# Performance work log

Measured on AMD Instinct MI355X. Metric: run time of the kernel, lower is better.

Reference implementation:

```python
import jax, jax.numpy as jnp
import numpy as np

TWO_PI = 6.283185307179586


def setup_inputs() -> dict:
    key = jax.random.key(0)
    k1, k2, k3, k4, k5, k6 = jax.random.split(key, 6)
    B, T, D = 2, 8192, 1024
    x = jax.random.normal(k1, (B, T, D), dtype=jnp.float32)
    # nn.Linear weights are [out, in]; init with small scale like torch default
    s = 1.0 / np.sqrt(D)
    Wk = jax.random.uniform(k2, (D, D), jnp.float32, -s, s)
    Wv = jax.random.uniform(k3, (D, D), jnp.float32, -s, s)
    Wo = jax.random.uniform(k4, (D, D), jnp.float32, -s, s)
    # random phasor frequencies in [0, 2*pi)
    freqs = jax.random.uniform(k5, (D,), jnp.float32, 0.0, TWO_PI)
    return {"x": x, "Wk": Wk, "Wv": Wv, "Wo": Wo, "freqs": freqs}


def reference(x, Wk, Wv, Wo, freqs):
    B, T, C = x.shape
    # k projection is computed in the original forward but never used downstream
    k_real = x @ Wk.T  # [B,T,D] (dead value, kept for fidelity)
    v_real = x @ Wv.T  # [B,T,D]
    v = v_real.astype(jnp.complex64)
    # rotors: per-position unit phasors exp(i * t * freqs), shape [T, D]
    t = jnp.arange(T, dtype=jnp.float32)
    rotors = jnp.exp(1j * (t[:, None] * freqs[None, :])).astype(jnp.complex64)
    # bind each value with its rotor and accumulate causally (O(N) memory trace)
    memory_trace = jnp.cumsum(v * rotors[None, :, :], axis=1)  # [B,T,D] complex64
    # retrieve by unbinding with the conjugate rotor; take the real component
    retrieved = jnp.real(memory_trace * jnp.conj(rotors)[None, :, :])  # [B,T,D]
    return retrieved @ Wo.T
```

## Files before the change

kernel.cpp:

```cpp
#include <hip/hip_runtime.h>
#include <hip/hip_bf16.h>


#define B_  2
#define T_  8192
#define D_  1024
#define BT_ 16384
#define CS_ 64
#define NCHUNK_ 128

typedef __attribute__((ext_vector_type(4))) float f32x4;
typedef __attribute__((ext_vector_type(8))) short bf16x8;

static __device__ inline unsigned short f2bf(float f) {
    union { float f; unsigned int u; } a;
    a.f = f;
    unsigned int u = a.u;
    return (unsigned short)((u + 0x7FFFu + ((u >> 16) & 1u)) >> 16);
}
static __device__ inline float bf2f(unsigned short h) {
    union { unsigned int u; float f; } a;
    a.u = ((unsigned int)h) << 16;
    return a.f;
}

__global__ __launch_bounds__(256) void cast_all(const float* __restrict__ x,
                                                const float* __restrict__ Wv,
                                                const float* __restrict__ Wo,
                                                unsigned short* __restrict__ xb,
                                                unsigned short* __restrict__ wvb,
                                                unsigned short* __restrict__ wob) {
    const int nx = BT_ * D_ / 4;
    const int nw = D_ * D_ / 4;
    int i = blockIdx.x * 256 + threadIdx.x;
    const float4* src;
    unsigned short* dst;
    int j;
    if (i < nx)            { src = (const float4*)x;  dst = xb;  j = i; }
    else if (i < nx + nw)  { src = (const float4*)Wv; dst = wvb; j = i - nx; }
    else                   { src = (const float4*)Wo; dst = wob; j = i - nx - nw; }
    float4 v = src[j];
    ushort4 o;
    o.x = f2bf(v.x); o.y = f2bf(v.y); o.z = f2bf(v.z); o.w = f2bf(v.w);
    ((ushort4*)dst)[j] = o;
}

template <bool BF16OUT>
__global__ __launch_bounds__(256) void gemm_bt(const short* __restrict__ A,
                                               const short* __restrict__ Bm,
                                               void* __restrict__ Cout,
                                               int M, int N, int K) {
    __shared__ short lds[8192];
    const int lane = threadIdx.x & 63;
    const int wave = threadIdx.x >> 6;
    const int wr = wave >> 1, wc = wave & 1;

    const int nb = N >> 7;
    const int id = blockIdx.x;
    const int xcd = id & 7;
    const int slot = id >> 3;
    const int bn = (slot % nb) * 128;
    const int bm = (xcd * ((M >> 7) >> 3) + slot / nb) * 128;

    const int r0 = lane >> 2;
    const int cb = lane & 3;

    const int m_base = wr * 64 + (lane & 15);
    const int n_base = wc * 64 + (lane & 15);
    const int k_off = (lane >> 4) * 8;

    f32x4 acc[4][4] = {};

    for (int k0 = 0; k0 < K; k0 += 32) {
#pragma unroll
        for (int cc = 0; cc < 2; ++cc) {
            const int chunk = wave * 2 + cc;
            const int row = chunk * 16 + r0;
            const short* ga = A + (size_t)(bm + row) * K + k0 + cb * 8;
            const short* gb = Bm + (size_t)(bn + row) * K + k0 + cb * 8;
            __builtin_amdgcn_global_load_lds(
                (const __attribute__((address_space(1))) void*)ga,
                (__attribute__((address_space(3))) void*)&lds[chunk * 512], 16, 0, 0);
            __builtin_amdgcn_global_load_lds(
                (const __attribute__((address_space(1))) void*)gb,
                (__attribute__((address_space(3))) void*)&lds[4096 + chunk * 512], 16, 0, 0);
        }
        __syncthreads();
        bf16x8 a[4], b[4];
#pragma unroll
        for (int i = 0; i < 4; ++i)
            a[i] = *(const bf16x8*)&lds[(m_base + i * 16) * 32 + k_off];
#pragma unroll
        for (int j = 0; j < 4; ++j)
            b[j] = *(const bf16x8*)&lds[4096 + (n_base + j * 16) * 32 + k_off];
#pragma unroll
        for (int i = 0; i < 4; ++i)
#pragma unroll
            for (int j = 0; j < 4; ++j)
                acc[i][j] = __builtin_amdgcn_mfma_f32_16x16x32_bf16(a[i], b[j], acc[i][j], 0, 0, 0);
        __syncthreads();
    }

    const int row0 = (lane >> 4) * 4;
#pragma unroll
    for (int i = 0; i < 4; ++i) {
#pragma unroll
        for (int j = 0; j < 4; ++j) {
            const int col = bn + wc * 64 + j * 16 + (lane & 15);
#pragma unroll
            for (int r = 0; r < 4; ++r) {
                const size_t row = bm + wr * 64 + i * 16 + row0 + r;
                if constexpr (BF16OUT)
                    ((unsigned short*)Cout)[row * N + col] = f2bf(acc[i][j][r]);
                else
                    ((float*)Cout)[row * N + col] = acc[i][j][r];
            }
        }
    }
}

__global__ __launch_bounds__(256) void scan_pass1(const unsigned short* __restrict__ v,
                                                  const float* __restrict__ freqs,
                                                  float* __restrict__ csum) {
    const int d0 = (blockIdx.x * 256 + threadIdx.x) * 2;
    const int chunk = blockIdx.y;
    const int b = blockIdx.z;
    const float2 f2 = *(const float2*)(freqs + d0);
    const int t0 = chunk * CS_;
    float s0, c0, s1, c1, sf0, cf0, sf1, cf1;
    sincosf((float)t0 * f2.x, &s0, &c0);
    sincosf((float)t0 * f2.y, &s1, &c1);
    sincosf(f2.x, &sf0, &cf0);
    sincosf(f2.y, &sf1, &cf1);
    float ar0 = 0.f, ai0 = 0.f, ar1 = 0.f, ai1 = 0.f;
    const unsigned int* vp = (const unsigned int*)(v + ((size_t)b * T_ + t0) * D_ + d0);
    for (int t = 0; t < CS_; ++t) {
        unsigned int w2 = *vp; vp += D_ / 2;
        float w0 = bf2f((unsigned short)w2);
        float w1 = bf2f((unsigned short)(w2 >> 16));
        ar0 = fmaf(w0, c0, ar0); ai0 = fmaf(w0, s0, ai0);
        ar1 = fmaf(w1, c1, ar1); ai1 = fmaf(w1, s1, ai1);
        float nc0 = c0 * cf0 - s0 * sf0, ns0 = s0 * cf0 + c0 * sf0;
        float nc1 = c1 * cf1 - s1 * sf1, ns1 = s1 * cf1 + c1 * sf1;
        c0 = nc0; s0 = ns0; c1 = nc1; s1 = ns1;
    }
    float4 o; o.x = ar0; o.y = ai0; o.z = ar1; o.w = ai1;
    *(float4*)(csum + (((size_t)b * NCHUNK_ + chunk) * D_ + d0) * 2) = o;
}

__global__ __launch_bounds__(256) void scan_pass2(float* __restrict__ csum) {
    const int g = blockIdx.x * 256 + threadIdx.x;
    const int b = g / D_;
    const int d = g % D_;
    float2* cs = (float2*)csum;
    const size_t base = (size_t)b * NCHUNK_ * D_ + d;
    float pr = 0.f, pi = 0.f;
    for (int cc = 0; cc < NCHUNK_; cc += 16) {
        float2 buf[16];
#pragma unroll
        for (int k = 0; k < 16; ++k) buf[k] = cs[base + (size_t)(cc + k) * D_];
#pragma unroll
        for (int k = 0; k < 16; ++k) {
            float r = buf[k].x, im = buf[k].y;
            buf[k] = make_float2(pr, pi);
            pr += r; pi += im;
        }
#pragma unroll
        for (int k = 0; k < 16; ++k) cs[base + (size_t)(cc + k) * D_] = buf[k];
    }
}

__global__ __launch_bounds__(256) void scan_pass3(const unsigned short* __restrict__ v,
                                                  const float* __restrict__ freqs,
                                                  const float* __restrict__ csum,
                                                  unsigned short* __restrict__ ret) {
    const int d0 = (blockIdx.x * 256 + threadIdx.x) * 2;
    const int chunk = blockIdx.y;
    const int b = blockIdx.z;
    const float2 f2 = *(const float2*)(freqs + d0);
    const float4 cs4 = *(const float4*)(csum + (((size_t)b * NCHUNK_ + chunk) * D_ + d0) * 2);
    float ar0 = cs4.x, ai0 = cs4.y, ar1 = cs4.z, ai1 = cs4.w;
    const int t0 = chunk * CS_;
    float s0, c0, s1, c1, sf0, cf0, sf1, cf1;
    sincosf((float)t0 * f2.x, &s0, &c0);
    sincosf((float)t0 * f2.y, &s1, &c1);
    sincosf(f2.x, &sf0, &cf0);
    sincosf(f2.y, &sf1, &cf1);
    const unsigned int* vp = (const unsigned int*)(v + ((size_t)b * T_ + t0) * D_ + d0);
    unsigned int* rp = (unsigned int*)(ret + ((size_t)b * T_ + t0) * D_ + d0);
    for (int t = 0; t < CS_; ++t) {
        unsigned int w2 = *vp; vp += D_ / 2;
        float w0 = bf2f((unsigned short)w2);
        float w1 = bf2f((unsigned short)(w2 >> 16));
        ar0 = fmaf(w0, c0, ar0); ai0 = fmaf(w0, s0, ai0);
        ar1 = fmaf(w1, c1, ar1); ai1 = fmaf(w1, s1, ai1);
        float o0 = ar0 * c0 + ai0 * s0;
        float o1 = ar1 * c1 + ai1 * s1;
        *rp = (unsigned int)f2bf(o0) | ((unsigned int)f2bf(o1) << 16);
        rp += D_ / 2;
        float nc0 = c0 * cf0 - s0 * sf0, ns0 = s0 * cf0 + c0 * sf0;
        float nc1 = c1 * cf1 - s1 * sf1, ns1 = s1 * cf1 + c1 * sf1;
        c0 = nc0; s0 = ns0; c1 = nc1; s1 = ns1;
    }
}

extern "C" void kernel_launch(void* const* d_in, const int* in_sizes, int n_in,
                              void* d_out, int out_size, void* d_ws, size_t ws_size,
                              hipStream_t stream) {
    const float* x     = (const float*)d_in[0];
    const float* Wv    = (const float*)d_in[2];
    const float* Wo    = (const float*)d_in[3];
    const float* freqs = (const float*)d_in[4];
    float* out = (float*)d_out;

    char* ws = (char*)d_ws;
    unsigned short* x_bf  = (unsigned short*)ws;
    unsigned short* Wv_bf = (unsigned short*)(ws + 33554432);
    unsigned short* Wo_bf = (unsigned short*)(ws + 35651584);
    unsigned short* ret   = (unsigned short*)(ws + 37748736);
    float*          csum  = (float*)(ws + 71303168);
    unsigned short* v_bf = (unsigned short*)d_out;

    cast_all<<<(BT_ * D_ / 4 + 2 * D_ * D_ / 4) / 256, 256, 0, stream>>>(
        x, Wv, Wo, x_bf, Wv_bf, Wo_bf);

    gemm_bt<true><<<(BT_ / 128) * (D_ / 128), 256, 0, stream>>>(
        (const short*)x_bf, (const short*)Wv_bf, (void*)v_bf, BT_, D_, D_);

    dim3 sgrid(D_ / 512, NCHUNK_, B_);
    scan_pass1<<<sgrid, 256, 0, stream>>>(v_bf, freqs, csum);
    scan_pass2<<<(B_ * D_) / 256, 256, 0, stream>>>(csum);
    scan_pass3<<<sgrid, 256, 0, stream>>>(v_bf, freqs, csum, ret);

    gemm_bt<false><<<(BT_ / 128) * (D_ / 128), 256, 0, stream>>>(
        (const short*)ret, (const short*)Wo_bf, (void*)out, BT_, D_, D_);
}
```

Measured before the change: 263.4 us.

## Swizzle GEMM LDS layout and vectorize chunked scan passes with smaller chunks

Applies an XOR swizzle to the LDS tile layout in the bf16 GEMM so fragment reads avoid bank conflicts, and precomputes global and LDS offsets outside the k loop. Rewrites scan passes 1 and 3 so each thread handles 8 contiguous channels with 16-byte loads and stores and batches 8 timesteps of loads. It also halves the chunk length and doubles the chunk count. This adds more per-thread registers and a larger chunk-sum buffer and pass-2 workload.

```diff
diff --git a/kernel.cpp b/kernel.cpp
--- a/kernel.cpp
+++ b/kernel.cpp
@@ -6,8 +6,8 @@
 #define T_  8192
 #define D_  1024
 #define BT_ 16384
-#define CS_ 64
-#define NCHUNK_ 128
+#define CS_ 32
+#define NCHUNK_ 256
 
 typedef __attribute__((ext_vector_type(4))) float f32x4;
 typedef __attribute__((ext_vector_type(8))) short bf16x8;
@@ -23,6 +23,7 @@
     a.u = ((unsigned int)h) << 16;
     return a.f;
 }
+static __device__ inline int fsw(int r) { return ((r & 3) + ((r >> 2) & 3)) & 3; }
 
 __global__ __launch_bounds__(256) void cast_all(const float* __restrict__ x,
                                                 const float* __restrict__ Wv,
@@ -65,9 +66,26 @@
     const int r0 = lane >> 2;
     const int cb = lane & 3;
 
-    const int m_base = wr * 64 + (lane & 15);
-    const int n_base = wc * 64 + (lane & 15);
-    const int k_off = (lane >> 4) * 8;
+    const short* ga[2];
+    const short* gb[2];
+#pragma unroll
+    for (int cc = 0; cc < 2; ++cc) {
+        const int chunk = wave * 2 + cc;
+        const int row = chunk * 16 + r0;
+        const int col = (cb ^ fsw(row)) * 8;
+        ga[cc] = A + (size_t)(bm + row) * K + col;
+        gb[cc] = Bm + (size_t)(bn + row) * K + col;
+    }
+
+    const int c4r = lane >> 4;
+    int aoff[4], boff[4];
+#pragma unroll
+    for (int i = 0; i < 4; ++i) {
+        const int m = wr * 64 + (lane & 15) + i * 16;
+        aoff[i] = m * 32 + ((c4r ^ fsw(m)) * 8);
+        const int n = wc * 64 + (lane & 15) + i * 16;
+        boff[i] = 4096 + n * 32 + ((c4r ^ fsw(n)) * 8);
+    }
 
     f32x4 acc[4][4] = {};
 
@@ -75,24 +93,19 @@
 #pragma unroll
         for (int cc = 0; cc < 2; ++cc) {
             const int chunk = wave * 2 + cc;
-            const int row = chunk * 16 + r0;
-            const short* ga = A + (size_t)(bm + row) * K + k0 + cb * 8;
-            const short* gb = Bm + (size_t)(bn + row) * K + k0 + cb * 8;
             __builtin_amdgcn_global_load_lds(
-                (const __attribute__((address_space(1))) void*)ga,
+                (const __attribute__((address_space(1))) void*)(ga[cc] + k0),
                 (__attribute__((address_space(3))) void*)&lds[chunk * 512], 16, 0, 0);
             __builtin_amdgcn_global_load_lds(
-                (const __attribute__((address_space(1))) void*)gb,
+                (const __attribute__((address_space(1))) void*)(gb[cc] + k0),
                 (__attribute__((address_space(3))) void*)&lds[4096 + chunk * 512], 16, 0, 0);
         }
         __syncthreads();
         bf16x8 a[4], b[4];
 #pragma unroll
-        for (int i = 0; i < 4; ++i)
-            a[i] = *(const bf16x8*)&lds[(m_base + i * 16) * 32 + k_off];
-#pragma unroll
-        for (int j = 0; j < 4; ++j)
-            b[j] = *(const bf16x8*)&lds[4096 + (n_base + j * 16) * 32 + k_off];
+        for (int i = 0; i < 4; ++i) a[i] = *(const bf16x8*)&lds[aoff[i]];
+#pragma unroll
+        for (int j = 0; j < 4; ++j) b[j] = *(const bf16x8*)&lds[boff[j]];
 #pragma unroll
         for (int i = 0; i < 4; ++i)
 #pragma unroll
@@ -122,30 +135,49 @@
 __global__ __launch_bounds__(256) void scan_pass1(const unsigned short* __restrict__ v,
                                                   const float* __restrict__ freqs,
                                                   float* __restrict__ csum) {
-    const int d0 = (blockIdx.x * 256 + threadIdx.x) * 2;
-    const int chunk = blockIdx.y;
-    const int b = blockIdx.z;
-    const float2 f2 = *(const float2*)(freqs + d0);
-    const int t0 = chunk * CS_;
-    float s0, c0, s1, c1, sf0, cf0, sf1, cf1;
-    sincosf((float)t0 * f2.x, &s0, &c0);
-    sincosf((float)t0 * f2.y, &s1, &c1);
-    sincosf(f2.x, &sf0, &cf0);
-    sincosf(f2.y, &sf1, &cf1);
-    float ar0 = 0.f, ai0 = 0.f, ar1 = 0.f, ai1 = 0.f;
-    const unsigned int* vp = (const unsigned int*)(v + ((size_t)b * T_ + t0) * D_ + d0);
-    for (int t = 0; t < CS_; ++t) {
-        unsigned int w2 = *vp; vp += D_ / 2;
-        float w0 = bf2f((unsigned short)w2);
-        float w1 = bf2f((unsigned short)(w2 >> 16));
-        ar0 = fmaf(w0, c0, ar0); ai0 = fmaf(w0, s0, ai0);
-        ar1 = fmaf(w1, c1, ar1); ai1 = fmaf(w1, s1, ai1);
-        float nc0 = c0 * cf0 - s0 * sf0, ns0 = s0 * cf0 + c0 * sf0;
-        float nc1 = c1 * cf1 - s1 * sf1, ns1 = s1 * cf1 + c1 * sf1;
-        c0 = nc0; s0 = ns0; c1 = nc1; s1 = ns1;
-    }
-    float4 o; o.x = ar0; o.y = ai0; o.z = ar1; o.w = ai1;
-    *(float4*)(csum + (((size_t)b * NCHUNK_ + chunk) * D_ + d0) * 2) = o;
+    const int tid = threadIdx.x;
+    const int chunk = blockIdx.x * 2 + (tid >> 7);
+    const int b = blockIdx.y;
+    const int d0 = (tid & 127) * 8;
+
+    float fr[8], s[8], c[8], sf[8], cf[8], ar[8] = {}, ai[8] = {};
+    {
+        float4 fA = *(const float4*)(freqs + d0);
+        float4 fB = *(const float4*)(freqs + d0 + 4);
+        fr[0] = fA.x; fr[1] = fA.y; fr[2] = fA.z; fr[3] = fA.w;
+        fr[4] = fB.x; fr[5] = fB.y; fr[6] = fB.z; fr[7] = fB.w;
+    }
+    const float t0f = (float)(chunk * CS_);
+#pragma unroll
+    for (int k = 0; k < 8; ++k) {
+        sincosf(t0f * fr[k], &s[k], &c[k]);
+        sincosf(fr[k], &sf[k], &cf[k]);
+    }
+    const uint4* vp = (const uint4*)(v + ((size_t)b * T_ + chunk * CS_) * D_ + d0);
+    for (int tb = 0; tb < CS_; tb += 8) {
+        uint4 w[8];
+#pragma unroll
+        for (int u = 0; u < 8; ++u) w[u] = vp[(size_t)(tb + u) * (D_ / 8)];
+#pragma unroll
+        for (int u = 0; u < 8; ++u) {
+            const unsigned int wd[4] = {w[u].x, w[u].y, w[u].z, w[u].w};
+#pragma unroll
+            for (int k = 0; k < 8; ++k) {
+                float wv = bf2f((unsigned short)(wd[k >> 1] >> ((k & 1) * 16)));
+                ar[k] = fmaf(wv, c[k], ar[k]);
+                ai[k] = fmaf(wv, s[k], ai[k]);
+                float nc = c[k] * cf[k] - s[k] * sf[k];
+                float ns = s[k] * cf[k] + c[k] * sf[k];
+                c[k] = nc; s[k] = ns;
+            }
+        }
+    }
+    float4* cp = (float4*)(csum + (((size_t)b * NCHUNK_ + chunk) * D_ + d0) * 2);
+#pragma unroll
+    for (int k = 0; k < 4; ++k) {
+        float4 o; o.x = ar[2 * k]; o.y = ai[2 * k]; o.z = ar[2 * k + 1]; o.w = ai[2 * k + 1];
+        cp[k] = o;
+    }
 }
 
 __global__ __launch_bounds__(256) void scan_pass2(float* __restrict__ csum) {
@@ -174,33 +206,61 @@
                                                   const float* __restrict__ freqs,
                                                   const float* __restrict__ csum,
                                                   unsigned short* __restrict__ ret) {
-    const int d0 = (blockIdx.x * 256 + threadIdx.x) * 2;
-    const int chunk = blockIdx.y;
-    const int b = blockIdx.z;
-    const float2 f2 = *(const float2*)(freqs + d0);
-    const float4 cs4 = *(const float4*)(csum + (((size_t)b * NCHUNK_ + chunk) * D_ + d0) * 2);
-    float ar0 = cs4.x, ai0 = cs4.y, ar1 = cs4.z, ai1 = cs4.w;
-    const int t0 = chunk * CS_;
-    float s0, c0, s1, c1, sf0, cf0, sf1, cf1;
-    sincosf((float)t0 * f2.x, &s0, &c0);
-    sincosf((float)t0 * f2.y, &s1, &c1);
-    sincosf(f2.x, &sf0, &cf0);
-    sincosf(f2.y, &sf1, &cf1);
-    const unsigned int* vp = (const unsigned int*)(v + ((size_t)b * T_ + t0) * D_ + d0);
-    unsigned int* rp = (unsigned int*)(ret + ((size_t)b * T_ + t0) * D_ + d0);
-    for (int t = 0; t < CS_; ++t) {
-        unsigned int w2 = *vp; vp += D_ / 2;
-        float w0 = bf2f((unsigned short)w2);
-        float w1 = bf2f((unsigned short)(w2 >> 16));
-        ar0 = fmaf(w0, c0, ar0); ai0 = fmaf(w0, s0, ai0);
-        ar1 = fmaf(w1, c1, ar1); ai1 = fmaf(w1, s1, ai1);
-        float o0 = ar0 * c0 + ai0 * s0;
-        float o1 = ar1 * c1 + ai1 * s1;
-        *rp = (unsigned int)f2bf(o0) | ((unsigned int)f2bf(o1) << 16);
-        rp += D_ / 2;
-        float nc0 = c0 * cf0 - s0 * sf0, ns0 = s0 * cf0 + c0 * sf0;
-        float nc1 = c1 * cf1 - s1 * sf1, ns1 = s1 * cf1 + c1 * sf1;
-        c0 = nc0; s0 = ns0; c1 = nc1; s1 = ns1;
+    const int tid = threadIdx.x;
+    const int chunk = blockIdx.x * 2 + (tid >> 7);
+    const int b = blockIdx.y;
+    const int d0 = (tid & 127) * 8;
+
+    float fr[8], s[8], c[8], sf[8], cf[8], ar[8], ai[8];
+    {
+        float4 fA = *(const float4*)(freqs + d0);
+        float4 fB = *(const float4*)(freqs + d0 + 4);
+        fr[0] = fA.x; fr[1] = fA.y; fr[2] = fA.z; fr[3] = fA.w;
+        fr[4] = fB.x; fr[5] = fB.y; fr[6] = fB.z; fr[7] = fB.w;
+    }
+    const float t0f = (float)(chunk * CS_);
+#pragma unroll
+    for (int k = 0; k < 8; ++k) {
+        sincosf(t0f * fr[k], &s[k], &c[k]);
+        sincosf(fr[k], &sf[k], &cf[k]);
+    }
+    {
+        const float4* cp = (const float4*)(csum + (((size_t)b * NCHUNK_ + chunk) * D_ + d0) * 2);
+#pragma unroll
+        for (int k = 0; k < 4; ++k) {
+            float4 o = cp[k];
+            ar[2 * k] = o.x; ai[2 * k] = o.y; ar[2 * k + 1] = o.z; ai[2 * k + 1] = o.w;
+        }
+    }
+    const uint4* vp = (const uint4*)(v + ((size_t)b * T_ + chunk * CS_) * D_ + d0);
+    uint4* rp = (uint4*)(ret + ((size_t)b * T_ + chunk * CS_) * D_ + d0);
+    for (int tb = 0; tb < CS_; tb += 8) {
+        uint4 w[8];
+#pragma unroll
+        for (int u = 0; u < 8; ++u) w[u] = vp[(size_t)(tb + u) * (D_ / 8)];
+#pragma unroll
+        for (int u = 0; u < 8; ++u) {
+            const unsigned int wd[4] = {w[u].x, w[u].y, w[u].z, w[u].w};
+            unsigned int od[4];
+#pragma unroll
+            for (int k = 0; k < 8; k += 2) {
+                float w0 = bf2f((unsigned short)(wd[k >> 1]));
+                float w1 = bf2f((unsigned short)(wd[k >> 1] >> 16));
+                ar[k] = fmaf(w0, c[k], ar[k]); ai[k] = fmaf(w0, s[k], ai[k]);
+                ar[k + 1] = fmaf(w1, c[k + 1], ar[k + 1]); ai[k + 1] = fmaf(w1, s[k + 1], ai[k + 1]);
+                float o0 = ar[k] * c[k] + ai[k] * s[k];
+                float o1 = ar[k + 1] * c[k + 1] + ai[k + 1] * s[k + 1];
+                od[k >> 1] = (unsigned int)f2bf(o0) | ((unsigned int)f2bf(o1) << 16);
+#pragma unroll
+                for (int q = 0; q < 2; ++q) {
+                    float nc = c[k + q] * cf[k + q] - s[k + q] * sf[k + q];
+                    float ns = s[k + q] * cf[k + q] + c[k + q] * sf[k + q];
+                    c[k + q] = nc; s[k + q] = ns;
+                }
+            }
+            uint4 o4; o4.x = od[0]; o4.y = od[1]; o4.z = od[2]; o4.w = od[3];
+            rp[(size_t)(tb + u) * (D_ / 8)] = o4;
+        }
     }
 }
 
@@ -227,7 +287,7 @@
     gemm_bt<true><<<(BT_ / 128) * (D_ / 128), 256, 0, stream>>>(
         (const short*)x_bf, (const short*)Wv_bf, (void*)v_bf, BT_, D_, D_);
 
-    dim3 sgrid(D_ / 512, NCHUNK_, B_);
+    dim3 sgrid(NCHUNK_ / 2, B_);
     scan_pass1<<<sgrid, 256, 0, stream>>>(v_bf, freqs, csum);
     scan_pass2<<<(B_ * D_) / 256, 256, 0, stream>>>(csum);
     scan_pass3<<<sgrid, 256, 0, stream>>>(v_bf, freqs, csum, ret);
```

Measured after the change: 282.0 us. 7.1% more time.
